# Optimization experiments

Hardware: AMD Instinct MI355X
Metric: run time of the kernel (lower is better)

## Reference

```python
import jax, jax.numpy as jnp
import numpy as np

B, S, H = 32, 512, 768
N, E, P = 4096, 131072, 65536
HEADS1, C1 = 4, 128
HEADS2, C2 = 1, 64
NUM_REL, REL_HID = 6, 256
NER_HID, NER_LAB = 256, 9
LRELU_SLOPE = 0.2  # PyG GATConv default negative_slope
LN_EPS = 1e-5


def setup_inputs() -> dict:
    key = jax.random.key(0)
    ks = jax.random.split(key, 24)
    sc = 0.02
    inp = {
        'sequence_output': jax.random.normal(ks[0], (B, S, H), jnp.float32),
        'ent_start': jax.random.randint(ks[1], (N,), 0, S - 8),
        'ent_len': jax.random.randint(ks[2], (N,), 0, 8),
        'ent_batch': jax.random.randint(ks[3], (N,), 0, B),
        'edge_index': jax.random.randint(ks[4], (2, E), 0, N),
        'pair_idx': jax.random.randint(ks[5], (P, 2), 0, N),
        'W1': jax.random.normal(ks[6], (H, HEADS1 * C1), jnp.float32) * sc,
        'a_src1': jax.random.normal(ks[7], (HEADS1, C1), jnp.float32) * sc,
        'a_dst1': jax.random.normal(ks[8], (HEADS1, C1), jnp.float32) * sc,
        'b1': jnp.zeros((HEADS1 * C1,), jnp.float32),
        'W2': jax.random.normal(ks[9], (HEADS1 * C1, HEADS2 * C2), jnp.float32) * sc,
        'a_src2': jax.random.normal(ks[10], (HEADS2, C2), jnp.float32) * sc,
        'a_dst2': jax.random.normal(ks[11], (HEADS2, C2), jnp.float32) * sc,
        'b2': jnp.zeros((HEADS2 * C2,), jnp.float32),
        # 6 per-relation classifiers: Linear(128,256)+LN+ReLU+Linear(256,1)
        'relW1': jax.random.normal(ks[12], (NUM_REL, 2 * C2, REL_HID), jnp.float32) * sc,
        'relb1': jnp.zeros((NUM_REL, REL_HID), jnp.float32),
        'ln_g': jnp.ones((NUM_REL, REL_HID), jnp.float32),
        'ln_b': jnp.zeros((NUM_REL, REL_HID), jnp.float32),
        'relW2': jax.random.normal(ks[13], (NUM_REL, REL_HID, 1), jnp.float32) * sc,
        'relb2': jnp.zeros((NUM_REL, 1), jnp.float32),
        # NER head: Linear(768,256)+ReLU+Linear(256,9)
        'nerW1': jax.random.normal(ks[14], (H, NER_HID), jnp.float32) * sc,
        'nerb1': jnp.zeros((NER_HID,), jnp.float32),
        'nerW2': jax.random.normal(ks[15], (NER_HID, NER_LAB), jnp.float32) * sc,
        'nerb2': jnp.zeros((NER_LAB,), jnp.float32),
    }
    return inp


def _gat(x, src, dst, W, a_src, a_dst, b, heads, ch, n):
    # PyG GATConv: per-head linear, additive attention, softmax over incoming edges
    h = (x @ W).reshape(n, heads, ch)                      # [N,Hd,C]
    e_src = jnp.sum(h * a_src, axis=-1)                    # [N,Hd]
    e_dst = jnp.sum(h * a_dst, axis=-1)
    e = jax.nn.leaky_relu(e_src[src] + e_dst[dst], LRELU_SLOPE)  # [E,Hd]
    m = jax.ops.segment_max(e, dst, num_segments=n)
    ex = jnp.exp(e - m[dst])
    denom = jax.ops.segment_sum(ex, dst, num_segments=n)
    alpha = ex / denom[dst]                                # [E,Hd]
    out = jax.ops.segment_sum(alpha[:, :, None] * h[src], dst, num_segments=n)
    return out.reshape(n, heads * ch) + b


def reference(sequence_output, ent_start, ent_len, ent_batch, edge_index, pair_idx,
              W1, a_src1, a_dst1, b1, W2, a_src2, a_dst2, b2,
              relW1, relb1, ln_g, ln_b, relW2, relb2,
              nerW1, nerb1, nerW2, nerb2):
    n = ent_start.shape[0]
    # NER head on the full sequence
    ner_logits = jax.nn.relu(sequence_output @ nerW1 + nerb1) @ nerW2 + nerb2  # [B,S,9]
    # Entity-span mean pooling via exclusive prefix sums (inclusive span start..start+len)
    csum = jnp.cumsum(sequence_output, axis=1)
    csum = jnp.concatenate([jnp.zeros((B, 1, H), sequence_output.dtype), csum], axis=1)  # [B,S+1,H]
    ent_end = ent_start + ent_len
    span_sum = csum[ent_batch, ent_end + 1] - csum[ent_batch, ent_start]  # [N,H]
    x = span_sum / (ent_len + 1).astype(span_sum.dtype)[:, None]
    # add self loops (PyG GATConv default add_self_loops=True)
    loops = jnp.arange(n, dtype=edge_index.dtype)
    src = jnp.concatenate([edge_index[0], loops])
    dst = jnp.concatenate([edge_index[1], loops])
    x = _gat(x, src, dst, W1, a_src1, a_dst1, b1, HEADS1, C1, n)
    x = jax.nn.relu(x)  # dropout p=0.3 is identity in eval mode
    x = _gat(x, src, dst, W2, a_src2, a_dst2, b2, HEADS2, C2, n)  # [N,64]
    # Pair features: cat(x[e1], x[e2]) -> [P,128]
    pair_feat = jnp.concatenate([x[pair_idx[:, 0]], x[pair_idx[:, 1]]], axis=-1)
    # All 6 relation classifiers, vectorized over the relation dim
    hid = jnp.einsum('pf,rfk->rpk', pair_feat, relW1) + relb1[:, None, :]  # [6,P,256]
    mu = jnp.mean(hid, axis=-1, keepdims=True)
    var = jnp.mean(jnp.square(hid - mu), axis=-1, keepdims=True)
    hid = (hid - mu) * jax.lax.rsqrt(var + LN_EPS) * ln_g[:, None, :] + ln_b[:, None, :]
    hid = jax.nn.relu(hid)
    rel_logits = (jnp.einsum('rpk,rko->rpo', hid, relW2) + relb2[:, None, :])[..., 0]  # [6,P]
    return ner_logits, rel_logits
```

## Files before the change

### kernel.cpp

```cpp
#include <hip/hip_runtime.h>
#include <math.h>

#define LRELU 0.2f

constexpr int Bn = 32, Sn = 512, Hn = 768, Nn = 4096, En = 131072, Pn = 65536;
constexpr int ET = En + Nn;

typedef __attribute__((ext_vector_type(8))) short bf16x8;
typedef __attribute__((ext_vector_type(4))) float f32x4;

constexpr size_t OFF_X0  = 0;
constexpr size_t OFF_UV  = 0;
constexpr size_t OFF_H1  = 4194304;
constexpr size_t OFF_X1  = OFF_H1  + 2097152;
constexpr size_t OFF_H2  = OFF_X1  + 2097152;
constexpr size_t OFF_X2  = OFF_H2  + 262144;
constexpr size_t OFF_ES1 = OFF_X2  + 262144;
constexpr size_t OFF_ED1 = OFF_ES1 + 16384;
constexpr size_t OFF_ES2 = OFF_ED1 + 16384;
constexpr size_t OFF_ED2 = OFF_ES2 + 4096;
constexpr size_t OFF_ROW = OFF_ED2 + 4096;
constexpr size_t OFF_CUR = OFF_ROW + 4104;
constexpr size_t OFF_EDG = OFF_CUR + 4096;
constexpr size_t OFF_W1S = OFF_EDG + 135168;
constexpr size_t OFF_NW1S = OFF_W1S + 196608;

__device__ __forceinline__ short f2bf(float f) {
  union { float f; unsigned u; } x; x.f = f;
  unsigned r = x.u + 0x7fff + ((x.u >> 16) & 1);
  return (short)(r >> 16);
}
__device__ __forceinline__ float bf2f(short s) {
  union { unsigned u; float f; } x;
  x.u = ((unsigned)(unsigned short)s) << 16;
  return x.f;
}

__global__ __launch_bounds__(256) void span_pool_k(
    const float* __restrict__ seq, const int* __restrict__ est,
    const int* __restrict__ eln, const int* __restrict__ ebt,
    float* __restrict__ x0) {
  int idx = blockIdx.x * 256 + threadIdx.x;
  if (idx >= Nn * (Hn / 4)) return;
  int e = idx / (Hn / 4);
  int c = (idx % (Hn / 4)) * 4;
  int s0 = est[e], L = eln[e] + 1, b = ebt[e];
  const float* p = seq + ((size_t)b * Sn + s0) * Hn + c;
  float ax = 0, ay = 0, az = 0, aw = 0;
  for (int i = 0; i < L; ++i) {
    float4 v = *(const float4*)(p + (size_t)i * Hn);
    ax += v.x; ay += v.y; az += v.z; aw += v.w;
  }
  float inv = 1.0f / (float)L;
  float4 o; o.x = ax * inv; o.y = ay * inv; o.z = az * inv; o.w = aw * inv;
  *(float4*)&x0[(size_t)e * Hn + c] = o;
}

template <int EPI, int NTW, int KC>
__global__ __launch_bounds__(256) void mfma_gemm_k(
    const float* __restrict__ A, const short* __restrict__ Bswz,
    float* __restrict__ C, const float* __restrict__ bias,
    int M, int K, int N) {
  constexpr int RS = KC + 8;
  __shared__ short at[64 * RS];
  int t = threadIdx.x;
  size_t rowb = (size_t)blockIdx.x * 64;
  int colb = blockIdx.y * (64 * NTW);
  int w = t >> 6, lane = t & 63, quad = lane >> 4, id = lane & 15;
  f32x4 acc[4][NTW];
#pragma unroll
  for (int mt = 0; mt < 4; ++mt)
#pragma unroll
    for (int nt = 0; nt < NTW; ++nt) acc[mt][nt] = (f32x4){0.f, 0.f, 0.f, 0.f};

  for (int k0 = 0; k0 < K; k0 += KC) {
    constexpr int CH = 64 * KC / 8 / 256;
#pragma unroll
    for (int i = 0; i < CH; ++i) {
      int cid = t + i * 256;
      int p = cid / (KC / 8), o8 = (cid % (KC / 8)) * 8;
      const float* src = &A[(rowb + p) * (size_t)K + k0 + o8];
      float4 v0 = *(const float4*)src;
      float4 v1 = *(const float4*)(src + 4);
      bf16x8 bv;
      bv[0] = f2bf(v0.x); bv[1] = f2bf(v0.y); bv[2] = f2bf(v0.z); bv[3] = f2bf(v0.w);
      bv[4] = f2bf(v1.x); bv[5] = f2bf(v1.y); bv[6] = f2bf(v1.z); bv[7] = f2bf(v1.w);
      *(bf16x8*)&at[p * RS + o8] = bv;
    }
    __syncthreads();
#pragma unroll
    for (int kk = 0; kk < KC / 32; ++kk) {
      bf16x8 af[4], bfr[NTW];
#pragma unroll
      for (int mt = 0; mt < 4; ++mt)
        af[mt] = *(const bf16x8*)&at[(mt * 16 + id) * RS + kk * 32 + quad * 8];
#pragma unroll
      for (int nt = 0; nt < NTW; ++nt) {
        int ntg = (colb >> 4) + w * NTW + nt;
        bfr[nt] = *(const bf16x8*)&Bswz[(((size_t)(k0 >> 5) + kk) * (N >> 4) + ntg) * 512 + lane * 8];
      }
#pragma unroll
      for (int mt = 0; mt < 4; ++mt)
#pragma unroll
        for (int nt = 0; nt < NTW; ++nt)
          acc[mt][nt] = __builtin_amdgcn_mfma_f32_16x16x32_bf16(af[mt], bfr[nt], acc[mt][nt], 0, 0, 0);
    }
    __syncthreads();
  }
#pragma unroll
  for (int nt = 0; nt < NTW; ++nt) {
    int col = colb + w * (16 * NTW) + nt * 16 + id;
    float bb = (EPI == 1) ? bias[col] : 0.f;
#pragma unroll
    for (int mt = 0; mt < 4; ++mt) {
#pragma unroll
      for (int reg = 0; reg < 4; ++reg) {
        size_t row = rowb + mt * 16 + quad * 4 + reg;
        float v = acc[mt][nt][reg];
        if (EPI == 1) v = fmaxf(v + bb, 0.f);
        if (EPI == 2) ((short*)C)[row * (size_t)N + col] = f2bf(v);
        else          C[row * (size_t)N + col] = v;
      }
    }
  }
}

template <int K, int N>
__global__ void swz_k(const float* __restrict__ B, short* __restrict__ o) {
  int i = blockIdx.x * 256 + threadIdx.x;
  if (i >= K * N) return;
  int n = i % N, k = i / N;
  int kk = k >> 5, quad = (k >> 3) & 3, j = k & 7, ntg = n >> 4, id = n & 15;
  o[(((size_t)kk * (N >> 4)) + ntg) * 512 + (quad * 16 + id) * 8 + j] = f2bf(B[i]);
}

__global__ void swz_uv_k(const float* __restrict__ rW1, short* __restrict__ o) {
  int i = blockIdx.x * 256 + threadIdx.x;
  if (i >= 6 * 128 * 256) return;
  int n = i & 255, k = (i >> 8) & 127, r = i >> 15;
  int c = r * 512 + (k >> 6) * 256 + n;
  int kr = k & 63;
  int kk = kr >> 5, quad = (kr >> 3) & 3, j = kr & 7, ntg = c >> 4, id = c & 15;
  o[(((size_t)kk * 192) + ntg) * 512 + (quad * 16 + id) * 8 + j] = f2bf(rW1[i]);
}

template <int HD, int C>
__global__ __launch_bounds__(256) void coef_k(
    const float* __restrict__ h, const float* __restrict__ a_src,
    const float* __restrict__ a_dst, float* __restrict__ es, float* __restrict__ ed) {
  int idx = blockIdx.x * 256 + threadIdx.x;
  if (idx >= Nn * HD) return;
  int n = idx / HD, hd = idx % HD;
  const float* hp = h + (size_t)n * HD * C + hd * C;
  const float* sp = a_src + hd * C;
  const float* dp = a_dst + hd * C;
  float s = 0, d = 0;
  for (int c = 0; c < C; c += 4) {
    float4 v = *(const float4*)(hp + c);
    float4 a = *(const float4*)(sp + c);
    float4 b = *(const float4*)(dp + c);
    s += v.x * a.x + v.y * a.y + v.z * a.z + v.w * a.w;
    d += v.x * b.x + v.y * b.y + v.z * b.z + v.w * b.w;
  }
  es[idx] = s; ed[idx] = d;
}

__global__ void zero_k(int* __restrict__ p, int n) {
  int i = blockIdx.x * 256 + threadIdx.x;
  if (i < n) p[i] = 0;
}

__global__ void count_k(const int* __restrict__ eidx, int* __restrict__ cnt) {
  int i = blockIdx.x * 256 + threadIdx.x;
  if (i >= ET) return;
  int dst = (i < En) ? eidx[En + i] : (i - En);
  atomicAdd(&cnt[dst], 1);
}

__global__ __launch_bounds__(256) void scan_k(int* cnt_cur, int* rowoff) {
  __shared__ int s[256];
  int t = threadIdx.x;
  int loc[16]; int run = 0; int base = t * 16;
#pragma unroll
  for (int i = 0; i < 16; ++i) { loc[i] = run; run += cnt_cur[base + i]; }
  s[t] = run;
  __syncthreads();
  for (int off = 1; off < 256; off <<= 1) {
    int v = (t >= off) ? s[t - off] : 0;
    __syncthreads();
    s[t] += v;
    __syncthreads();
  }
  int offset = (t > 0) ? s[t - 1] : 0;
#pragma unroll
  for (int i = 0; i < 16; ++i) {
    int o = offset + loc[i];
    rowoff[base + i] = o;
    cnt_cur[base + i] = o;
  }
  if (t == 255) rowoff[4096] = s[255];
}

__global__ void scatter_k(const int* __restrict__ eidx, int* __restrict__ cur,
                          int* __restrict__ esrc) {
  int i = blockIdx.x * 256 + threadIdx.x;
  if (i >= ET) return;
  int s, d;
  if (i < En) { s = eidx[i]; d = eidx[En + i]; } else { s = d = i - En; }
  int pos = atomicAdd(&cur[d], 1);
  esrc[pos] = s;
}

template <int HD, int C, bool RELU>
__global__ __launch_bounds__(256) void gat_agg_k(
    const float* __restrict__ h, const float* __restrict__ es,
    const float* __restrict__ ed, const int* __restrict__ row_off,
    const int* __restrict__ eslist, const float* __restrict__ bias,
    float* __restrict__ xout) {
  constexpr int CAP = 320;
  __shared__ float red[256];
  __shared__ float mxs[HD], dns[HD];
  __shared__ float exc[CAP * HD];
  int n = blockIdx.x, t = threadIdx.x;
  int ro = row_off[n], deg = row_off[n + 1] - ro;
  int hd = t % HD, ei = t / HD;
  constexpr int ES = 256 / HD;
  float edv = ed[n * HD + hd];
  float pm = -3.402823466e38f;
  for (int j = ei; j < deg; j += ES) {
    int s = eslist[ro + j];
    float e = es[s * HD + hd] + edv;
    e = (e > 0.f) ? e : LRELU * e;
    pm = fmaxf(pm, e);
  }
  red[t] = pm;
  __syncthreads();
  for (int off = 128; off >= HD; off >>= 1) {
    if (t < off) red[t] = fmaxf(red[t], red[t + off]);
    __syncthreads();
  }
  if (t < HD) mxs[t] = red[t];
  __syncthreads();
  float mx = mxs[hd];
  float ps = 0.f;
  for (int j = ei; j < deg; j += ES) {
    int s = eslist[ro + j];
    float e = es[s * HD + hd] + edv;
    e = (e > 0.f) ? e : LRELU * e;
    float ex = __expf(e - mx);
    if (j < CAP) exc[j * HD + hd] = ex;
    ps += ex;
  }
  red[t] = ps;
  __syncthreads();
  for (int off = 128; off >= HD; off >>= 1) {
    if (t < off) red[t] += red[t + off];
    __syncthreads();
  }
  if (t < HD) dns[t] = red[t];
  __syncthreads();
  for (int c = t; c < HD * C; c += 256) {
    int hh = c / C;
    float mxh = mxs[hh], edh = ed[n * HD + hh];
    float acc = 0.f;
    for (int j = 0; j < deg; ++j) {
      int s = eslist[ro + j];
      float ex;
      if (j < CAP) ex = exc[j * HD + hh];
      else {
        float e = es[s * HD + hh] + edh;
        e = (e > 0.f) ? e : LRELU * e;
        ex = __expf(e - mxh);
      }
      acc += ex * h[(size_t)s * (HD * C) + c];
    }
    float v = acc / dns[hh] + bias[c];
    if (RELU) v = fmaxf(v, 0.f);
    xout[(size_t)n * (HD * C) + c] = v;
  }
}

__global__ __launch_bounds__(256) void pair_rel_k(
    const short* __restrict__ UV, const int* __restrict__ pidx,
    const float* __restrict__ rb1, const float* __restrict__ lng,
    const float* __restrict__ lnb, const float* __restrict__ rW2,
    const float* __restrict__ rb2, float* __restrict__ out) {
  int t = threadIdx.x;
  int r = blockIdx.y;
  int w = t >> 6, lane = t & 63;
  int pg = lane >> 4, l16 = lane & 15;
  float rbl[16], g[16], bb[16], wv[16];
  int cb = r * 256 + l16 * 16;
#pragma unroll
  for (int q = 0; q < 4; ++q) {
    *(float4*)&rbl[q * 4] = *(const float4*)&rb1[cb + q * 4];
    *(float4*)&g[q * 4]   = *(const float4*)&lng[cb + q * 4];
    *(float4*)&bb[q * 4]  = *(const float4*)&lnb[cb + q * 4];
    *(float4*)&wv[q * 4]  = *(const float4*)&rW2[cb + q * 4];
  }
  float rb2v = rb2[r];
  int pbase = blockIdx.x * 256 + w * 64;
  for (int it = 0; it < 16; ++it) {
    int p = pbase + it * 4 + pg;
    int i = pidx[p * 2], j = pidx[p * 2 + 1];
    const short* up = &UV[(size_t)i * 3072 + r * 512 + l16 * 16];
    const short* vp = &UV[(size_t)j * 3072 + r * 512 + 256 + l16 * 16];
    bf16x8 u0 = *(const bf16x8*)up, u1 = *(const bf16x8*)(up + 8);
    bf16x8 v0 = *(const bf16x8*)vp, v1 = *(const bf16x8*)(vp + 8);
    float hv[16], s1 = 0.f, s2 = 0.f;
#pragma unroll
    for (int cc = 0; cc < 8; ++cc) {
      float h = bf2f(u0[cc]) + bf2f(v0[cc]) + rbl[cc];
      hv[cc] = h; s1 += h; s2 += h * h;
    }
#pragma unroll
    for (int cc = 0; cc < 8; ++cc) {
      float h = bf2f(u1[cc]) + bf2f(v1[cc]) + rbl[8 + cc];
      hv[8 + cc] = h; s1 += h; s2 += h * h;
    }
#pragma unroll
    for (int off = 1; off < 16; off <<= 1) {
      s1 += __shfl_xor(s1, off, 64);
      s2 += __shfl_xor(s2, off, 64);
    }
    float mu = s1 * (1.f / 256.f);
    float var = s2 * (1.f / 256.f) - mu * mu;
    float rs = rsqrtf(var + 1e-5f);
    float pv = 0.f;
#pragma unroll
    for (int cc = 0; cc < 16; ++cc) {
      float v = (hv[cc] - mu) * rs * g[cc] + bb[cc];
      v = fmaxf(v, 0.f);
      pv += v * wv[cc];
    }
#pragma unroll
    for (int off = 1; off < 16; off <<= 1) pv += __shfl_xor(pv, off, 64);
    if (l16 == 0) out[(size_t)r * Pn + p] = pv + rb2v;
  }
}

__global__ __launch_bounds__(256) void ner2_k(
    const float* __restrict__ hid, const float* __restrict__ W2,
    const float* __restrict__ b2, float* __restrict__ out) {
  __shared__ float s[16 * 257];
  int t = threadIdx.x;
  int rowb = blockIdx.x * 16;
#pragma unroll
  for (int i = 0; i < 4; ++i) {
    int cid = t + i * 256;
    int r = cid >> 6;
    int c4 = (cid & 63) * 4;
    *(float4*)&s[r * 257 + c4] = *(const float4*)&hid[(size_t)(rowb + r) * 256 + c4];
  }
  __syncthreads();
  int r = t & 15, j = t >> 4;
  if (j < 9) {
    float a = 0.f;
    for (int k = 0; k < 256; ++k) a += s[r * 257 + k] * W2[k * 9 + j];
    out[(size_t)(rowb + r) * 9 + j] = a + b2[j];
  }
}

extern "C" void kernel_launch(void* const* d_in, const int* in_sizes, int n_in,
                              void* d_out, int out_size, void* d_ws, size_t ws_size,
                              hipStream_t stream) {
  const float* seq = (const float*)d_in[0];
  const int* est = (const int*)d_in[1];
  const int* eln = (const int*)d_in[2];
  const int* ebt = (const int*)d_in[3];
  const int* eidx = (const int*)d_in[4];
  const int* pidx = (const int*)d_in[5];
  const float* W1 = (const float*)d_in[6];
  const float* as1 = (const float*)d_in[7];
  const float* ad1 = (const float*)d_in[8];
  const float* b1 = (const float*)d_in[9];
  const float* W2 = (const float*)d_in[10];
  const float* as2 = (const float*)d_in[11];
  const float* ad2 = (const float*)d_in[12];
  const float* b2 = (const float*)d_in[13];
  const float* rW1 = (const float*)d_in[14];
  const float* rb1 = (const float*)d_in[15];
  const float* lng = (const float*)d_in[16];
  const float* lnb = (const float*)d_in[17];
  const float* rW2 = (const float*)d_in[18];
  const float* rb2 = (const float*)d_in[19];
  const float* nW1 = (const float*)d_in[20];
  const float* nb1 = (const float*)d_in[21];
  const float* nW2 = (const float*)d_in[22];
  const float* nb2 = (const float*)d_in[23];
  float* out = (float*)d_out;
  float* ws = (float*)d_ws;

  float* x0 = ws + OFF_X0;
  short* uv = (short*)(ws + OFF_UV);
  float* h1 = ws + OFF_H1;
  float* x1 = ws + OFF_X1;
  float* h2 = ws + OFF_H2;
  short* uvw = (short*)(ws + OFF_H2);
  float* x2 = ws + OFF_X2;
  float* es1 = ws + OFF_ES1;
  float* ed1 = ws + OFF_ED1;
  float* es2 = ws + OFF_ES2;
  float* ed2 = ws + OFF_ED2;
  int* rowoff = (int*)(ws + OFF_ROW);
  int* cur = (int*)(ws + OFF_CUR);
  int* edg = (int*)(ws + OFF_EDG);
  short* w1s = (short*)(ws + OFF_W1S);
  short* w2s = (short*)(ws + OFF_W1S);
  short* nw1s = (short*)(ws + OFF_NW1S);
  float* nhid = ws + OFF_X0;

  zero_k<<<16, 256, 0, stream>>>(cur, Nn);
  count_k<<<(ET + 255) / 256, 256, 0, stream>>>(eidx, cur);
  scan_k<<<1, 256, 0, stream>>>(cur, rowoff);
  scatter_k<<<(ET + 255) / 256, 256, 0, stream>>>(eidx, cur, edg);
  swz_k<768, 512><<<(768 * 512 + 255) / 256, 256, 0, stream>>>(W1, w1s);
  swz_k<768, 256><<<(768 * 256 + 255) / 256, 256, 0, stream>>>(nW1, nw1s);

  span_pool_k<<<Nn * (Hn / 4) / 256, 256, 0, stream>>>(seq, est, eln, ebt, x0);

  mfma_gemm_k<0, 2, 128><<<dim3(Nn / 64, 512 / 128), 256, 0, stream>>>(x0, w1s, h1, nullptr, Nn, Hn, 512);
  swz_k<512, 64><<<(512 * 64 + 255) / 256, 256, 0, stream>>>(W2, w2s);
  coef_k<4, 128><<<(Nn * 4) / 256, 256, 0, stream>>>(h1, as1, ad1, es1, ed1);
  gat_agg_k<4, 128, true><<<Nn, 256, 0, stream>>>(h1, es1, ed1, rowoff, edg, b1, x1);

  mfma_gemm_k<0, 1, 128><<<dim3(Nn / 64, 1), 256, 0, stream>>>(x1, w2s, h2, nullptr, Nn, 512, 64);
  coef_k<1, 64><<<(Nn + 255) / 256, 256, 0, stream>>>(h2, as2, ad2, es2, ed2);
  gat_agg_k<1, 64, false><<<Nn, 256, 0, stream>>>(h2, es2, ed2, rowoff, edg, b2, x2);

  swz_uv_k<<<(6 * 128 * 256) / 256, 256, 0, stream>>>(rW1, uvw);
  mfma_gemm_k<2, 2, 64><<<dim3(Nn / 64, 3072 / 128), 256, 0, stream>>>(x2, uvw, (float*)uv, nullptr, Nn, 64, 3072);
  pair_rel_k<<<dim3(Pn / 256, 6), 256, 0, stream>>>(uv, pidx, rb1, lng, lnb, rW2, rb2,
                                                    out + (size_t)Bn * Sn * 9);

  mfma_gemm_k<1, 2, 128><<<dim3((Bn * Sn) / 64, 256 / 128), 256, 0, stream>>>(seq, nw1s, nhid, nb1, Bn * Sn, Hn, 256);
  ner2_k<<<(Bn * Sn) / 16, 256, 0, stream>>>(nhid, nW2, nb2, out);
}
```

Measured before the change: 375.6 us.

## Fuse NER MLP into one kernel and group pair classifier by first entity

The NER head's two linear layers are fused into one kernel: the hidden activations stay in shared memory as bf16 and the 9-way projection runs there, so the 16384x256 fp32 hidden tensor is no longer written to and re-read from global memory. The pair relation kernel is restructured around a CSR grouping of pairs by their first entity, built with count, scan and scatter passes, so each wave loads the U row once and reuses it across all pairs sharing that entity. This adds four small launches and atomics, and makes wave workload depend on per-entity degree, which leaves partly idle lanes when degree is not a multiple of 4. The hidden activation is also rounded to bf16 before the second NER layer.

```diff
diff --git a/kernel.cpp b/kernel.cpp
--- a/kernel.cpp
+++ b/kernel.cpp
@@ -110,18 +110,103 @@
 #pragma unroll
   for (int nt = 0; nt < NTW; ++nt) {
     int col = colb + w * (16 * NTW) + nt * 16 + id;
-    float bb = (EPI == 1) ? bias[col] : 0.f;
 #pragma unroll
     for (int mt = 0; mt < 4; ++mt) {
 #pragma unroll
       for (int reg = 0; reg < 4; ++reg) {
         size_t row = rowb + mt * 16 + quad * 4 + reg;
         float v = acc[mt][nt][reg];
-        if (EPI == 1) v = fmaxf(v + bb, 0.f);
         if (EPI == 2) ((short*)C)[row * (size_t)N + col] = f2bf(v);
         else          C[row * (size_t)N + col] = v;
       }
     }
+  }
+}
+
+__global__ __launch_bounds__(256) void ner_fused_k(
+    const float* __restrict__ A, const short* __restrict__ Bswz,
+    const float* __restrict__ W2, const float* __restrict__ b1,
+    const float* __restrict__ b2, float* __restrict__ out) {
+  constexpr int K = 768, N = 256;
+  constexpr int RS = 136, HS = 264, WS = 260;
+  __shared__ short at[64 * RS];
+  __shared__ short hid[64 * HS];
+  __shared__ float w2t[9 * WS];
+  __shared__ float b2l[9];
+  int t = threadIdx.x;
+  size_t rowb = (size_t)blockIdx.x * 64;
+  for (int u = t; u < 2304; u += 256) {
+    int k = u / 9, jj = u % 9;
+    w2t[jj * WS + k] = W2[u];
+  }
+  if (t < 9) b2l[t] = b2[t];
+  int w = t >> 6, lane = t & 63, quad = lane >> 4, id = lane & 15;
+  f32x4 acc[4][4];
+#pragma unroll
+  for (int mt = 0; mt < 4; ++mt)
+#pragma unroll
+    for (int nt = 0; nt < 4; ++nt) acc[mt][nt] = (f32x4){0.f, 0.f, 0.f, 0.f};
+
+  for (int k0 = 0; k0 < K; k0 += 128) {
+#pragma unroll
+    for (int i = 0; i < 4; ++i) {
+      int cid = t + i * 256;
+      int p = cid >> 4, o8 = (cid & 15) * 8;
+      const float* src = &A[(rowb + p) * (size_t)K + k0 + o8];
+      float4 v0 = *(const float4*)src;
+      float4 v1 = *(const float4*)(src + 4);
+      bf16x8 bv;
+      bv[0] = f2bf(v0.x); bv[1] = f2bf(v0.y); bv[2] = f2bf(v0.z); bv[3] = f2bf(v0.w);
+      bv[4] = f2bf(v1.x); bv[5] = f2bf(v1.y); bv[6] = f2bf(v1.z); bv[7] = f2bf(v1.w);
+      *(bf16x8*)&at[p * RS + o8] = bv;
+    }
+    __syncthreads();
+#pragma unroll
+    for (int kk = 0; kk < 4; ++kk) {
+      bf16x8 af[4], bfr[4];
+#pragma unroll
+      for (int mt = 0; mt < 4; ++mt)
+        af[mt] = *(const bf16x8*)&at[(mt * 16 + id) * RS + kk * 32 + quad * 8];
+#pragma unroll
+      for (int nt = 0; nt < 4; ++nt) {
+        int ntg = w * 4 + nt;
+        bfr[nt] = *(const bf16x8*)&Bswz[(((size_t)(k0 >> 5) + kk) * 16 + ntg) * 512 + lane * 8];
+      }
+#pragma unroll
+      for (int mt = 0; mt < 4; ++mt)
+#pragma unroll
+        for (int nt = 0; nt < 4; ++nt)
+          acc[mt][nt] = __builtin_amdgcn_mfma_f32_16x16x32_bf16(af[mt], bfr[nt], acc[mt][nt], 0, 0, 0);
+    }
+    __syncthreads();
+  }
+#pragma unroll
+  for (int nt = 0; nt < 4; ++nt) {
+    int col = w * 64 + nt * 16 + id;
+    float bb = b1[col];
+#pragma unroll
+    for (int mt = 0; mt < 4; ++mt)
+#pragma unroll
+      for (int reg = 0; reg < 4; ++reg) {
+        int row = mt * 16 + quad * 4 + reg;
+        hid[row * HS + col] = f2bf(fmaxf(acc[mt][nt][reg] + bb, 0.f));
+      }
+  }
+  __syncthreads();
+  for (int u = t; u < 576; u += 256) {
+    int row = u / 9, jj = u % 9;
+    const short* hp = &hid[row * HS];
+    const float* wp = &w2t[jj * WS];
+    float a = 0.f;
+#pragma unroll
+    for (int k8 = 0; k8 < 256; k8 += 8) {
+      bf16x8 hv = *(const bf16x8*)&hp[k8];
+      float4 w0 = *(const float4*)&wp[k8];
+      float4 w1 = *(const float4*)&wp[k8 + 4];
+      a += bf2f(hv[0]) * w0.x + bf2f(hv[1]) * w0.y + bf2f(hv[2]) * w0.z + bf2f(hv[3]) * w0.w;
+      a += bf2f(hv[4]) * w1.x + bf2f(hv[5]) * w1.y + bf2f(hv[6]) * w1.z + bf2f(hv[7]) * w1.w;
+    }
+    out[(rowb + row) * 9 + jj] = a + b2l[jj];
   }
 }
 
@@ -209,6 +294,20 @@
   if (i < En) { s = eidx[i]; d = eidx[En + i]; } else { s = d = i - En; }
   int pos = atomicAdd(&cur[d], 1);
   esrc[pos] = s;
+}
+
+__global__ void pcount_k(const int* __restrict__ pidx, int* __restrict__ cnt) {
+  int p = blockIdx.x * 256 + threadIdx.x;
+  if (p < Pn) atomicAdd(&cnt[pidx[2 * p]], 1);
+}
+
+__global__ void pscatter_k(const int* __restrict__ pidx, int* __restrict__ cur,
+                           int2* __restrict__ plist) {
+  int p = blockIdx.x * 256 + threadIdx.x;
+  if (p >= Pn) return;
+  int i = pidx[2 * p];
+  int pos = atomicAdd(&cur[i], 1);
+  plist[pos] = make_int2(pidx[2 * p + 1], p);
 }
 
 template <int HD, int C, bool RELU>
@@ -280,17 +379,19 @@
   }
 }
 
-__global__ __launch_bounds__(256) void pair_rel_k(
-    const short* __restrict__ UV, const int* __restrict__ pidx,
-    const float* __restrict__ rb1, const float* __restrict__ lng,
-    const float* __restrict__ lnb, const float* __restrict__ rW2,
-    const float* __restrict__ rb2, float* __restrict__ out) {
+__global__ __launch_bounds__(256) void pair_rel2_k(
+    const short* __restrict__ UV, const int* __restrict__ prow,
+    const int2* __restrict__ plist, const float* __restrict__ rb1,
+    const float* __restrict__ lng, const float* __restrict__ lnb,
+    const float* __restrict__ rW2, const float* __restrict__ rb2,
+    float* __restrict__ out) {
   int t = threadIdx.x;
   int r = blockIdx.y;
   int w = t >> 6, lane = t & 63;
   int pg = lane >> 4, l16 = lane & 15;
+  int n = blockIdx.x * 4 + w;
+  int cb = r * 256 + l16 * 16;
   float rbl[16], g[16], bb[16], wv[16];
-  int cb = r * 256 + l16 * 16;
 #pragma unroll
   for (int q = 0; q < 4; ++q) {
     *(float4*)&rbl[q * 4] = *(const float4*)&rb1[cb + q * 4];
@@ -299,23 +400,30 @@
     *(float4*)&wv[q * 4]  = *(const float4*)&rW2[cb + q * 4];
   }
   float rb2v = rb2[r];
-  int pbase = blockIdx.x * 256 + w * 64;
-  for (int it = 0; it < 16; ++it) {
-    int p = pbase + it * 4 + pg;
-    int i = pidx[p * 2], j = pidx[p * 2 + 1];
-    const short* up = &UV[(size_t)i * 3072 + r * 512 + l16 * 16];
-    const short* vp = &UV[(size_t)j * 3072 + r * 512 + 256 + l16 * 16];
-    bf16x8 u0 = *(const bf16x8*)up, u1 = *(const bf16x8*)(up + 8);
+  const short* up = &UV[(size_t)n * 3072 + r * 512 + l16 * 16];
+  bf16x8 u0 = *(const bf16x8*)up, u1 = *(const bf16x8*)(up + 8);
+  float ur[16];
+#pragma unroll
+  for (int cc = 0; cc < 8; ++cc) {
+    ur[cc] = bf2f(u0[cc]) + rbl[cc];
+    ur[8 + cc] = bf2f(u1[cc]) + rbl[8 + cc];
+  }
+  int ro = prow[n], deg = prow[n + 1] - ro;
+  for (int base = 0; base < deg; base += 4) {
+    int slot = base + pg;
+    bool act = slot < deg;
+    int2 jp = act ? plist[ro + slot] : make_int2(0, 0);
+    const short* vp = &UV[(size_t)jp.x * 3072 + r * 512 + 256 + l16 * 16];
     bf16x8 v0 = *(const bf16x8*)vp, v1 = *(const bf16x8*)(vp + 8);
     float hv[16], s1 = 0.f, s2 = 0.f;
 #pragma unroll
     for (int cc = 0; cc < 8; ++cc) {
-      float h = bf2f(u0[cc]) + bf2f(v0[cc]) + rbl[cc];
+      float h = ur[cc] + bf2f(v0[cc]);
       hv[cc] = h; s1 += h; s2 += h * h;
     }
 #pragma unroll
     for (int cc = 0; cc < 8; ++cc) {
-      float h = bf2f(u1[cc]) + bf2f(v1[cc]) + rbl[8 + cc];
+      float h = ur[8 + cc] + bf2f(v1[cc]);
       hv[8 + cc] = h; s1 += h; s2 += h * h;
     }
 #pragma unroll
@@ -335,29 +443,7 @@
     }
 #pragma unroll
     for (int off = 1; off < 16; off <<= 1) pv += __shfl_xor(pv, off, 64);
-    if (l16 == 0) out[(size_t)r * Pn + p] = pv + rb2v;
-  }
-}
-
-__global__ __launch_bounds__(256) void ner2_k(
-    const float* __restrict__ hid, const float* __restrict__ W2,
-    const float* __restrict__ b2, float* __restrict__ out) {
-  __shared__ float s[16 * 257];
-  int t = threadIdx.x;
-  int rowb = blockIdx.x * 16;
-#pragma unroll
-  for (int i = 0; i < 4; ++i) {
-    int cid = t + i * 256;
-    int r = cid >> 6;
-    int c4 = (cid & 63) * 4;
-    *(float4*)&s[r * 257 + c4] = *(const float4*)&hid[(size_t)(rowb + r) * 256 + c4];
-  }
-  __syncthreads();
-  int r = t & 15, j = t >> 4;
-  if (j < 9) {
-    float a = 0.f;
-    for (int k = 0; k < 256; ++k) a += s[r * 257 + k] * W2[k * 9 + j];
-    out[(size_t)(rowb + r) * 9 + j] = a + b2[j];
+    if (l16 == 0 && act) out[(size_t)r * Pn + jp.y] = pv + rb2v;
   }
 }
 
@@ -408,7 +494,9 @@
   short* w1s = (short*)(ws + OFF_W1S);
   short* w2s = (short*)(ws + OFF_W1S);
   short* nw1s = (short*)(ws + OFF_NW1S);
-  float* nhid = ws + OFF_X0;
+  int* prow = (int*)(ws + OFF_X1);
+  int* pcur = (int*)(ws + OFF_X1 + 4104);
+  int2* plist = (int2*)(ws + OFF_X1 + 8208);
 
   zero_k<<<16, 256, 0, stream>>>(cur, Nn);
   count_k<<<(ET + 255) / 256, 256, 0, stream>>>(eidx, cur);
@@ -425,14 +513,19 @@
   gat_agg_k<4, 128, true><<<Nn, 256, 0, stream>>>(h1, es1, ed1, rowoff, edg, b1, x1);
 
   mfma_gemm_k<0, 1, 128><<<dim3(Nn / 64, 1), 256, 0, stream>>>(x1, w2s, h2, nullptr, Nn, 512, 64);
+
+  zero_k<<<16, 256, 0, stream>>>(pcur, Nn);
+  pcount_k<<<Pn / 256, 256, 0, stream>>>(pidx, pcur);
+  scan_k<<<1, 256, 0, stream>>>(pcur, prow);
+  pscatter_k<<<Pn / 256, 256, 0, stream>>>(pidx, pcur, plist);
+
   coef_k<1, 64><<<(Nn + 255) / 256, 256, 0, stream>>>(h2, as2, ad2, es2, ed2);
   gat_agg_k<1, 64, false><<<Nn, 256, 0, stream>>>(h2, es2, ed2, rowoff, edg, b2, x2);
 
   swz_uv_k<<<(6 * 128 * 256) / 256, 256, 0, stream>>>(rW1, uvw);
   mfma_gemm_k<2, 2, 64><<<dim3(Nn / 64, 3072 / 128), 256, 0, stream>>>(x2, uvw, (float*)uv, nullptr, Nn, 64, 3072);
-  pair_rel_k<<<dim3(Pn / 256, 6), 256, 0, stream>>>(uv, pidx, rb1, lng, lnb, rW2, rb2,
-                                                    out + (size_t)Bn * Sn * 9);
-
-  mfma_gemm_k<1, 2, 128><<<dim3((Bn * Sn) / 64, 256 / 128), 256, 0, stream>>>(seq, nw1s, nhid, nb1, Bn * Sn, Hn, 256);
-  ner2_k<<<(Bn * Sn) / 16, 256, 0, stream>>>(nhid, nW2, nb2, out);
-}
+  pair_rel2_k<<<dim3(Nn / 4, 6), 256, 0, stream>>>(uv, prow, plist, rb1, lng, lnb, rW2, rb2,
+                                                   out + (size_t)Bn * Sn * 9);
+
+  ner_fused_k<<<(Bn * Sn) / 64, 256, 0, stream>>>(seq, nw1s, nW2, nb1, nb2, out);
+}
```

Result: slower. 395.6 us (+5.3%).
